# Kernel tuning notes

Measured on AMD Instinct MI355X. Metric: run time of the kernel, lower is better.

The kernel has to match this reference:

```python
import jax, jax.numpy as jnp
import numpy as np

NEG_BIG = -9e15


def setup_inputs() -> dict:
    key = jax.random.key(0)
    k1, k2, k3, k4 = jax.random.split(key, 4)
    B, N, F_in, F_out = 8, 2048, 512, 256
    x = jax.random.normal(k1, (B, N, F_in), dtype=jnp.float32)
    adj = jax.random.randint(k2, (B, N, N), 0, 2, dtype=jnp.int32)
    W = jax.random.normal(k3, (F_in, F_out), dtype=jnp.float32) * (1.414 / np.sqrt(F_in))
    a = jax.random.normal(k4, (2 * F_out, 1), dtype=jnp.float32) * 0.1
    return {"x": x, "adj": adj, "W": W, "a": a}


def reference(x, adj, W, a):
    # x: [B,N,Fin], adj: [B,N,N] int mask, W: [Fin,Fout], a: [2*Fout,1]
    alpha = 0.2  # LeakyReLU negative slope
    F_out = W.shape[1]
    h = jnp.einsum('bnf,fo->bno', x, W)              # [B,N,Fout]
    a1 = a[:F_out, 0]                                # [Fout]
    a2 = a[F_out:, 0]                                # [Fout]
    # e_ij = LeakyReLU([h_i || h_j] . a) = LeakyReLU(h_i.a1 + h_j.a2)
    f = h @ a1                                       # [B,N]
    g = h @ a2                                       # [B,N]
    e = jax.nn.leaky_relu(f[:, :, None] + g[:, None, :], negative_slope=alpha)  # [B,N,N]
    e = jnp.where(adj > 0, e, NEG_BIG)
    attention = jax.nn.softmax(e, axis=2)            # row-wise over neighbors j
    h_prime = jnp.einsum('bij,bjo->bio', attention, h)  # [B,N,Fout]
    return jax.nn.elu(h_prime)                       # concat=True path
```

## Files before the change

### kernel.cpp

```cpp
#include <hip/hip_runtime.h>
#include <math.h>

#define BATCH 8
#define NN    2048
#define FIN   512
#define FOUT  256
#define NEG_BIG -9000000000000000.0f

typedef __attribute__((ext_vector_type(8))) short bf16x8;
typedef __attribute__((ext_vector_type(4))) float f32x4;

__device__ __forceinline__ unsigned short f2bf(float x) {
    unsigned u = __float_as_uint(x);
    u = (u + 0x7FFF + ((u >> 16) & 1)) >> 16;
    return (unsigned short)u;
}
__device__ __forceinline__ float bf2f(unsigned short h) {
    return __uint_as_float(((unsigned)h) << 16);
}
__device__ __forceinline__ void gload_lds16(const void* g, void* l) {
    __builtin_amdgcn_global_load_lds((const __attribute__((address_space(1))) void*)g,
                                     (__attribute__((address_space(3))) void*)l,
                                     16, 0, 0);
}

__global__ __launch_bounds__(256) void wt_prep(const float* __restrict__ W,
                                               unsigned short* __restrict__ Wt_hi,
                                               unsigned short* __restrict__ Wt_lo) {
    const int tg = blockIdx.x * 256 + threadIdx.x;
    const int n  = tg >> 7;
    const int k4 = (tg & 127) * 4;
    unsigned short h[4], lo[4];
    #pragma unroll
    for (int i = 0; i < 4; i++) {
        const float v = W[(size_t)(k4 + i) * FOUT + n];
        h[i]  = f2bf(v);
        lo[i] = f2bf(v - bf2f(h[i]));
    }
    uint2 ph, pl;
    ph.x = h[0]  | ((unsigned)h[1]  << 16); ph.y = h[2]  | ((unsigned)h[3]  << 16);
    pl.x = lo[0] | ((unsigned)lo[1] << 16); pl.y = lo[2] | ((unsigned)lo[3] << 16);
    *(uint2*)(Wt_hi + (size_t)n * FIN + k4) = ph;
    *(uint2*)(Wt_lo + (size_t)n * FIN + k4) = pl;
}

__global__ __launch_bounds__(256, 2) void gemm_xw(const float* __restrict__ x,
        const unsigned short* __restrict__ Wt_hi,
        const unsigned short* __restrict__ Wt_lo,
        unsigned short* __restrict__ ht_hi,
        unsigned short* __restrict__ ht_lo) {
    __shared__ unsigned short As_hi[128][40];
    __shared__ unsigned short As_lo[128][40];
    __shared__ __attribute__((aligned(16))) unsigned short Tr[64][136];
    const int t  = threadIdx.x;
    const int m0 = (blockIdx.x >> 2) * 128;
    const int n0 = (blockIdx.x & 3) * 64;
    const int l  = t & 63, w = t >> 6;
    const int wr = w >> 1, wc = w & 1;
    const int lr = l & 15, lk = l >> 4;

    f32x4 acc[4][2];
    #pragma unroll
    for (int mt = 0; mt < 4; mt++)
        #pragma unroll
        for (int nt = 0; nt < 2; nt++) acc[mt][nt] = (f32x4){0.f,0.f,0.f,0.f};

    for (int k0 = 0; k0 < FIN; k0 += 32) {
        float4 xv[4];
        #pragma unroll
        for (int r = 0; r < 4; r++) {
            const int fidx = t + 256*r, m = fidx >> 3, kq = fidx & 7;
            xv[r] = *(const float4*)(x + (size_t)(m0 + m) * FIN + k0 + kq*4);
        }
        bf16x8 bh[2], bl[2];
        #pragma unroll
        for (int nt = 0; nt < 2; nt++) {
            const size_t off = (size_t)(n0 + wc*32 + nt*16 + lr) * FIN + k0 + lk*8;
            bh[nt] = *(const bf16x8*)(Wt_hi + off);
            bl[nt] = *(const bf16x8*)(Wt_lo + off);
        }
        __syncthreads();
        #pragma unroll
        for (int r = 0; r < 4; r++) {
            const int fidx = t + 256*r, m = fidx >> 3, kq = fidx & 7;
            const float vv[4] = {xv[r].x, xv[r].y, xv[r].z, xv[r].w};
            unsigned short h[4], lo[4];
            #pragma unroll
            for (int i = 0; i < 4; i++) { h[i] = f2bf(vv[i]); lo[i] = f2bf(vv[i] - bf2f(h[i])); }
            uint2 ph, pl;
            ph.x = h[0]  | ((unsigned)h[1]  << 16); ph.y = h[2]  | ((unsigned)h[3]  << 16);
            pl.x = lo[0] | ((unsigned)lo[1] << 16); pl.y = lo[2] | ((unsigned)lo[3] << 16);
            *(uint2*)&As_hi[m][kq*4] = ph;
            *(uint2*)&As_lo[m][kq*4] = pl;
        }
        __syncthreads();
        bf16x8 ah[4], al[4];
        #pragma unroll
        for (int mt = 0; mt < 4; mt++) {
            const int row = wr*64 + mt*16 + lr;
            ah[mt] = *(const bf16x8*)&As_hi[row][lk*8];
            al[mt] = *(const bf16x8*)&As_lo[row][lk*8];
        }
        #pragma unroll
        for (int nt = 0; nt < 2; nt++)
            #pragma unroll
            for (int mt = 0; mt < 4; mt++)
                acc[mt][nt] = __builtin_amdgcn_mfma_f32_16x16x32_bf16(ah[mt], bh[nt], acc[mt][nt], 0, 0, 0);
        #pragma unroll
        for (int nt = 0; nt < 2; nt++)
            #pragma unroll
            for (int mt = 0; mt < 4; mt++)
                acc[mt][nt] = __builtin_amdgcn_mfma_f32_16x16x32_bf16(ah[mt], bl[nt], acc[mt][nt], 0, 0, 0);
        #pragma unroll
        for (int nt = 0; nt < 2; nt++)
            #pragma unroll
            for (int mt = 0; mt < 4; mt++)
                acc[mt][nt] = __builtin_amdgcn_mfma_f32_16x16x32_bf16(al[mt], bh[nt], acc[mt][nt], 0, 0, 0);
    }

    const int bb  = m0 >> 11;
    const int jj0 = m0 & 2047;
    for (int pass = 0; pass < 2; pass++) {
        #pragma unroll
        for (int mt = 0; mt < 4; mt++)
            #pragma unroll
            for (int nt = 0; nt < 2; nt++) {
                const int nl = wc*32 + nt*16 + lr;
                const int ml = wr*64 + mt*16 + lk*4;
                const float vv[4] = {acc[mt][nt].x, acc[mt][nt].y, acc[mt][nt].z, acc[mt][nt].w};
                unsigned short s[4];
                #pragma unroll
                for (int r = 0; r < 4; r++) {
                    const unsigned short hh = f2bf(vv[r]);
                    s[r] = pass ? f2bf(vv[r] - bf2f(hh)) : hh;
                }
                *(unsigned*)&Tr[nl][ml]     = s[0] | ((unsigned)s[1] << 16);
                *(unsigned*)&Tr[nl][ml + 2] = s[2] | ((unsigned)s[3] << 16);
            }
        __syncthreads();
        unsigned short* dst = pass ? ht_lo : ht_hi;
        #pragma unroll
        for (int q = 0; q < 4; q++) {
            const int idx = t + 256*q, row = idx >> 4, c = idx & 15;
            *(uint4*)(dst + ((size_t)(bb * FOUT + n0 + row)) * NN + jj0 + c*8) =
                *(const uint4*)&Tr[row][c*8];
        }
        __syncthreads();
    }
}

__global__ __launch_bounds__(256) void fg2(const unsigned short* __restrict__ ht_hi,
                                           const unsigned short* __restrict__ ht_lo,
                                           const float* __restrict__ a,
                                           float* __restrict__ f, float* __restrict__ g) {
    const int lane  = threadIdx.x & 63;
    const int chunk = blockIdx.x * 4 + (threadIdx.x >> 6);
    const int b  = chunk >> 5;
    const int jw = (chunk & 31) * 64 + lane;
    const size_t base = (size_t)b * FOUT * NN + jw;
    float fs = 0.f, gs = 0.f;
    #pragma unroll 4
    for (int n = 0; n < FOUT; n++) {
        const float hv = bf2f(ht_hi[base + (size_t)n * NN]) + bf2f(ht_lo[base + (size_t)n * NN]);
        fs = fmaf(hv, a[n], fs);
        gs = fmaf(hv, a[FOUT + n], gs);
    }
    f[b * NN + jw] = fs;
    g[b * NN + jw] = gs;
}

__global__ __launch_bounds__(512, 1) void gat_attn(
        const unsigned short* __restrict__ ht_hi,
        const unsigned short* __restrict__ ht_lo,
        const int* __restrict__ adj,
        const float* __restrict__ f, const float* __restrict__ g,
        float* __restrict__ out) {
    __shared__ __attribute__((aligned(16))) unsigned short Hs_hi[256*64];
    __shared__ __attribute__((aligned(16))) unsigned short Hs_lo[256*64];
    __shared__ __attribute__((aligned(16))) unsigned short Ps_hi[64*64];
    __shared__ __attribute__((aligned(16))) unsigned short Ps_lo[64*64];
    __shared__ __attribute__((aligned(16))) float m_s[64];
    __shared__ __attribute__((aligned(16))) float l_s[64];
    __shared__ __attribute__((aligned(16))) float fac_s[64];

    const int b  = blockIdx.x & 7;
    const int i0 = (blockIdx.x >> 3) * 64;
    const int t  = threadIdx.x;
    const int w  = t >> 6, l = t & 63;
    const int lr = l & 15, lk = l >> 4;
    const int wr = w >> 2, wc = w & 3;
    const int ar = t >> 3, jg = t & 7;

    const float fi = f[b * NN + i0 + ar];
    if (t < 64) { m_s[t] = -INFINITY; l_s[t] = 0.f; }

    f32x4 acc[2][4];
    #pragma unroll
    for (int mt = 0; mt < 2; mt++)
        #pragma unroll
        for (int nt = 0; nt < 4; nt++) acc[mt][nt] = (f32x4){0.f,0.f,0.f,0.f};

    const unsigned short* hb_hi = ht_hi + (size_t)b * FOUT * NN;
    const unsigned short* hb_lo = ht_lo + (size_t)b * FOUT * NN;
    const size_t arow = ((size_t)b * NN + i0 + ar) * NN + jg * 8;
    const float* grow = g + b * NN + jg * 8;

    int4   adjA = *(const int4*)(adj + arow);
    int4   adjB = *(const int4*)(adj + arow + 4);
    float4 gA   = *(const float4*)(grow);
    float4 gB   = *(const float4*)(grow + 4);

    const int sidx = w * 4;

    for (int jt = 0; jt < 32; jt++) {
        __syncthreads();

        const int j0 = jt * 64;
        #pragma unroll
        for (int q = 0; q < 4; q++) {
            const int idx = (sidx + q) * 64 + l;
            const int n = idx >> 3, c = idx & 7;
            const int cc = c ^ (n & 7);
            const size_t go = (size_t)n * NN + j0 + cc * 8;
            gload_lds16(hb_hi + go, &Hs_hi[(sidx + q) * 512]);
            gload_lds16(hb_lo + go, &Hs_lo[(sidx + q) * 512]);
        }

        {
            float s[8];
            {
                const float v0 = fi + gA.x, v1 = fi + gA.y, v2 = fi + gA.z, v3 = fi + gA.w;
                const float v4 = fi + gB.x, v5 = fi + gB.y, v6 = fi + gB.z, v7 = fi + gB.w;
                s[0] = adjA.x > 0 ? (v0 > 0.f ? v0 : 0.2f*v0) : NEG_BIG;
                s[1] = adjA.y > 0 ? (v1 > 0.f ? v1 : 0.2f*v1) : NEG_BIG;
                s[2] = adjA.z > 0 ? (v2 > 0.f ? v2 : 0.2f*v2) : NEG_BIG;
                s[3] = adjA.w > 0 ? (v3 > 0.f ? v3 : 0.2f*v3) : NEG_BIG;
                s[4] = adjB.x > 0 ? (v4 > 0.f ? v4 : 0.2f*v4) : NEG_BIG;
                s[5] = adjB.y > 0 ? (v5 > 0.f ? v5 : 0.2f*v5) : NEG_BIG;
                s[6] = adjB.z > 0 ? (v6 > 0.f ? v6 : 0.2f*v6) : NEG_BIG;
                s[7] = adjB.w > 0 ? (v7 > 0.f ? v7 : 0.2f*v7) : NEG_BIG;
            }
            float mloc = s[0];
            #pragma unroll
            for (int e = 1; e < 8; e++) mloc = fmaxf(mloc, s[e]);
            mloc = fmaxf(mloc, __shfl_xor(mloc, 1));
            mloc = fmaxf(mloc, __shfl_xor(mloc, 2));
            mloc = fmaxf(mloc, __shfl_xor(mloc, 4));
            const float m_old = m_s[ar];
            const float m_new = fmaxf(m_old, mloc);
            float p[8], rs = 0.f;
            #pragma unroll
            for (int e = 0; e < 8; e++) { p[e] = __expf(s[e] - m_new); rs += p[e]; }
            rs += __shfl_xor(rs, 1);
            rs += __shfl_xor(rs, 2);
            rs += __shfl_xor(rs, 4);
            if (jg == 0) {
                const float fac = __expf(m_old - m_new);
                fac_s[ar] = fac;
                l_s[ar]   = l_s[ar] * fac + rs;
                m_s[ar]   = m_new;
            }
            unsigned ph[4], pl[4];
            #pragma unroll
            for (int e = 0; e < 8; e += 2) {
                const unsigned short h0 = f2bf(p[e]),   h1 = f2bf(p[e+1]);
                const unsigned short q0 = f2bf(p[e] - bf2f(h0));
                const unsigned short q1 = f2bf(p[e+1] - bf2f(h1));
                ph[e >> 1] = h0 | ((unsigned)h1 << 16);
                pl[e >> 1] = q0 | ((unsigned)q1 << 16);
            }
            const int cs = (jg ^ (ar & 7)) * 8;
            *(uint4*)&Ps_hi[ar * 64 + cs] = make_uint4(ph[0], ph[1], ph[2], ph[3]);
            *(uint4*)&Ps_lo[ar * 64 + cs] = make_uint4(pl[0], pl[1], pl[2], pl[3]);
        }
        __syncthreads();

        if (jt + 1 < 32) {
            const size_t o = (size_t)(jt + 1) * 64;
            adjA = *(const int4*)(adj + arow + o);
            adjB = *(const int4*)(adj + arow + o + 4);
            gA   = *(const float4*)(grow + o);
            gB   = *(const float4*)(grow + o + 4);
        }

        #pragma unroll
        for (int mt = 0; mt < 2; mt++) {
            const f32x4 fac4 = *(const f32x4*)&fac_s[wr*32 + mt*16 + lk*4];
            #pragma unroll
            for (int nt = 0; nt < 4; nt++) acc[mt][nt] *= fac4;
        }
        #pragma unroll
        for (int kt = 0; kt < 2; kt++) {
            bf16x8 ah[2], al[2], bh[4], bl[4];
            #pragma unroll
            for (int mt = 0; mt < 2; mt++) {
                const int row = wr*32 + mt*16 + lr;
                const int cs  = ((kt*4 + lk) ^ (row & 7)) * 8;
                ah[mt] = *(const bf16x8*)&Ps_hi[row * 64 + cs];
                al[mt] = *(const bf16x8*)&Ps_lo[row * 64 + cs];
            }
            #pragma unroll
            for (int nt = 0; nt < 4; nt++) {
                const int n  = wc*64 + nt*16 + lr;
                const int cs = ((kt*4 + lk) ^ (n & 7)) * 8;
                bh[nt] = *(const bf16x8*)&Hs_hi[n * 64 + cs];
                bl[nt] = *(const bf16x8*)&Hs_lo[n * 64 + cs];
            }
            #pragma unroll
            for (int nt = 0; nt < 4; nt++)
                #pragma unroll
                for (int mt = 0; mt < 2; mt++)
                    acc[mt][nt] = __builtin_amdgcn_mfma_f32_16x16x32_bf16(ah[mt], bh[nt], acc[mt][nt], 0, 0, 0);
            #pragma unroll
            for (int nt = 0; nt < 4; nt++)
                #pragma unroll
                for (int mt = 0; mt < 2; mt++)
                    acc[mt][nt] = __builtin_amdgcn_mfma_f32_16x16x32_bf16(ah[mt], bl[nt], acc[mt][nt], 0, 0, 0);
            #pragma unroll
            for (int nt = 0; nt < 4; nt++)
                #pragma unroll
                for (int mt = 0; mt < 2; mt++)
                    acc[mt][nt] = __builtin_amdgcn_mfma_f32_16x16x32_bf16(al[mt], bh[nt], acc[mt][nt], 0, 0, 0);
        }
    }

    __syncthreads();
    #pragma unroll
    for (int mt = 0; mt < 2; mt++) {
        const f32x4 lv = *(const f32x4*)&l_s[wr*32 + mt*16 + lk*4];
        const float linv[4] = {1.f/lv.x, 1.f/lv.y, 1.f/lv.z, 1.f/lv.w};
        #pragma unroll
        for (int nt = 0; nt < 4; nt++) {
            const int n = wc*64 + nt*16 + lr;
            const float av[4] = {acc[mt][nt].x, acc[mt][nt].y, acc[mt][nt].z, acc[mt][nt].w};
            #pragma unroll
            for (int r = 0; r < 4; r++) {
                float v = av[r] * linv[r];
                v = v > 0.f ? v : (__expf(v) - 1.f);
                out[((size_t)(b * NN + i0 + wr*32 + mt*16 + lk*4 + r)) * FOUT + n] = v;
            }
        }
    }
}

extern "C" void kernel_launch(void* const* d_in, const int* in_sizes, int n_in,
                              void* d_out, int out_size, void* d_ws, size_t ws_size,
                              hipStream_t stream) {
    const float* x   = (const float*)d_in[0];
    const int*   adj = (const int*)  d_in[1];
    const float* W   = (const float*)d_in[2];
    const float* a   = (const float*)d_in[3];
    float* outp = (float*)d_out;

    char* ws = (char*)d_ws;
    unsigned short* ht_hi = (unsigned short*)ws;                       ws += (size_t)BATCH*FOUT*NN*2;
    unsigned short* ht_lo = (unsigned short*)ws;                       ws += (size_t)BATCH*FOUT*NN*2;
    unsigned short* Wt_hi = (unsigned short*)ws;                       ws += (size_t)FOUT*FIN*2;
    unsigned short* Wt_lo = (unsigned short*)ws;                       ws += (size_t)FOUT*FIN*2;
    float* f = (float*)ws;                                             ws += (size_t)BATCH*NN*4;
    float* g = (float*)ws;

    wt_prep <<<128, 256, 0, stream>>>(W, Wt_hi, Wt_lo);
    gemm_xw <<<512, 256, 0, stream>>>(x, Wt_hi, Wt_lo, ht_hi, ht_lo);
    fg2     <<<64,  256, 0, stream>>>(ht_hi, ht_lo, a, f, g);
    gat_attn<<<256, 512, 0, stream>>>(ht_hi, ht_lo, adj, f, g, outp);
}
```

Baseline: 320.5 us.

## Compute softmax probabilities in MFMA registers and double-buffer H tiles

The attention kernel now has each wave compute the masked LeakyReLU scores and online-softmax probabilities directly in the MFMA A-operand register layout. This removes the P tile in shared memory, the shared max/sum/scale arrays and one barrier per tile. The H tile is double-buffered so the next tile's global-to-LDS load overlaps current compute, and adjacency/g loads are prefetched. The fg2 kernel splits the feature reduction across four waves with an LDS combine and launches more blocks for parallelism. Each of the four waves sharing a row block now redundantly computes the same probabilities and reads the same adjacency rows, which adds ALU work and adj traffic.

```diff
diff --git a/kernel.cpp b/kernel.cpp
--- a/kernel.cpp
+++ b/kernel.cpp
@@ -153,20 +153,25 @@
                                            const unsigned short* __restrict__ ht_lo,
                                            const float* __restrict__ a,
                                            float* __restrict__ f, float* __restrict__ g) {
-    const int lane  = threadIdx.x & 63;
-    const int chunk = blockIdx.x * 4 + (threadIdx.x >> 6);
+    __shared__ float Fp[4][64], Gp[4][64];
+    const int lane = threadIdx.x & 63, wv = threadIdx.x >> 6;
+    const int chunk = blockIdx.x;
     const int b  = chunk >> 5;
     const int jw = (chunk & 31) * 64 + lane;
     const size_t base = (size_t)b * FOUT * NN + jw;
     float fs = 0.f, gs = 0.f;
     #pragma unroll 4
-    for (int n = 0; n < FOUT; n++) {
+    for (int n = wv*64; n < wv*64 + 64; n++) {
         const float hv = bf2f(ht_hi[base + (size_t)n * NN]) + bf2f(ht_lo[base + (size_t)n * NN]);
         fs = fmaf(hv, a[n], fs);
         gs = fmaf(hv, a[FOUT + n], gs);
     }
-    f[b * NN + jw] = fs;
-    g[b * NN + jw] = gs;
+    Fp[wv][lane] = fs; Gp[wv][lane] = gs;
+    __syncthreads();
+    if (wv == 0) {
+        f[b * NN + jw] = Fp[0][lane] + Fp[1][lane] + Fp[2][lane] + Fp[3][lane];
+        g[b * NN + jw] = Gp[0][lane] + Gp[1][lane] + Gp[2][lane] + Gp[3][lane];
+    }
 }
 
 __global__ __launch_bounds__(512, 1) void gat_attn(
@@ -175,13 +180,8 @@
         const int* __restrict__ adj,
         const float* __restrict__ f, const float* __restrict__ g,
         float* __restrict__ out) {
-    __shared__ __attribute__((aligned(16))) unsigned short Hs_hi[256*64];
-    __shared__ __attribute__((aligned(16))) unsigned short Hs_lo[256*64];
-    __shared__ __attribute__((aligned(16))) unsigned short Ps_hi[64*64];
-    __shared__ __attribute__((aligned(16))) unsigned short Ps_lo[64*64];
-    __shared__ __attribute__((aligned(16))) float m_s[64];
-    __shared__ __attribute__((aligned(16))) float l_s[64];
-    __shared__ __attribute__((aligned(16))) float fac_s[64];
+    __shared__ __attribute__((aligned(16))) unsigned short Hs_hi[2][16384];
+    __shared__ __attribute__((aligned(16))) unsigned short Hs_lo[2][16384];
 
     const int b  = blockIdx.x & 7;
     const int i0 = (blockIdx.x >> 3) * 64;
@@ -189,153 +189,161 @@
     const int w  = t >> 6, l = t & 63;
     const int lr = l & 15, lk = l >> 4;
     const int wr = w >> 2, wc = w & 3;
-    const int ar = t >> 3, jg = t & 7;
-
-    const float fi = f[b * NN + i0 + ar];
-    if (t < 64) { m_s[t] = -INFINITY; l_s[t] = 0.f; }
-
-    f32x4 acc[2][4];
-    #pragma unroll
-    for (int mt = 0; mt < 2; mt++)
-        #pragma unroll
-        for (int nt = 0; nt < 4; nt++) acc[mt][nt] = (f32x4){0.f,0.f,0.f,0.f};
 
     const unsigned short* hb_hi = ht_hi + (size_t)b * FOUT * NN;
     const unsigned short* hb_lo = ht_lo + (size_t)b * FOUT * NN;
-    const size_t arow = ((size_t)b * NN + i0 + ar) * NN + jg * 8;
-    const float* grow = g + b * NN + jg * 8;
-
-    int4   adjA = *(const int4*)(adj + arow);
-    int4   adjB = *(const int4*)(adj + arow + 4);
-    float4 gA   = *(const float4*)(grow);
-    float4 gB   = *(const float4*)(grow + 4);
-
-    const int sidx = w * 4;
-
-    for (int jt = 0; jt < 32; jt++) {
-        __syncthreads();
-
+
+    const int rbase = i0 + wr*32 + lr;
+    const float fi0 = f[b*NN + rbase];
+    const float fi1 = f[b*NN + rbase + 16];
+    const int* adjr0 = adj + ((size_t)(b*NN + rbase)) * NN;
+    const int* adjr1 = adjr0 + (size_t)16 * NN;
+    const float* gb = g + b*NN;
+
+    float m_reg[2] = {-INFINITY, -INFINITY};
+    float l_reg[2] = {0.f, 0.f};
+    f32x4 acc[2][4] = {};
+
+    const int slot = w * 4;
+
+    int4   ap[2][2][2];
+    float4 gp[2][2];
+
+    auto STAGE = [&](int jt, int buf) {
         const int j0 = jt * 64;
         #pragma unroll
         for (int q = 0; q < 4; q++) {
-            const int idx = (sidx + q) * 64 + l;
+            const int idx = (slot + q) * 64 + l;
             const int n = idx >> 3, c = idx & 7;
             const int cc = c ^ (n & 7);
             const size_t go = (size_t)n * NN + j0 + cc * 8;
-            gload_lds16(hb_hi + go, &Hs_hi[(sidx + q) * 512]);
-            gload_lds16(hb_lo + go, &Hs_lo[(sidx + q) * 512]);
-        }
-
-        {
-            float s[8];
-            {
-                const float v0 = fi + gA.x, v1 = fi + gA.y, v2 = fi + gA.z, v3 = fi + gA.w;
-                const float v4 = fi + gB.x, v5 = fi + gB.y, v6 = fi + gB.z, v7 = fi + gB.w;
-                s[0] = adjA.x > 0 ? (v0 > 0.f ? v0 : 0.2f*v0) : NEG_BIG;
-                s[1] = adjA.y > 0 ? (v1 > 0.f ? v1 : 0.2f*v1) : NEG_BIG;
-                s[2] = adjA.z > 0 ? (v2 > 0.f ? v2 : 0.2f*v2) : NEG_BIG;
-                s[3] = adjA.w > 0 ? (v3 > 0.f ? v3 : 0.2f*v3) : NEG_BIG;
-                s[4] = adjB.x > 0 ? (v4 > 0.f ? v4 : 0.2f*v4) : NEG_BIG;
-                s[5] = adjB.y > 0 ? (v5 > 0.f ? v5 : 0.2f*v5) : NEG_BIG;
-                s[6] = adjB.z > 0 ? (v6 > 0.f ? v6 : 0.2f*v6) : NEG_BIG;
-                s[7] = adjB.w > 0 ? (v7 > 0.f ? v7 : 0.2f*v7) : NEG_BIG;
-            }
-            float mloc = s[0];
-            #pragma unroll
-            for (int e = 1; e < 8; e++) mloc = fmaxf(mloc, s[e]);
-            mloc = fmaxf(mloc, __shfl_xor(mloc, 1));
-            mloc = fmaxf(mloc, __shfl_xor(mloc, 2));
-            mloc = fmaxf(mloc, __shfl_xor(mloc, 4));
-            const float m_old = m_s[ar];
-            const float m_new = fmaxf(m_old, mloc);
-            float p[8], rs = 0.f;
-            #pragma unroll
-            for (int e = 0; e < 8; e++) { p[e] = __expf(s[e] - m_new); rs += p[e]; }
-            rs += __shfl_xor(rs, 1);
-            rs += __shfl_xor(rs, 2);
-            rs += __shfl_xor(rs, 4);
-            if (jg == 0) {
-                const float fac = __expf(m_old - m_new);
-                fac_s[ar] = fac;
-                l_s[ar]   = l_s[ar] * fac + rs;
-                m_s[ar]   = m_new;
-            }
-            unsigned ph[4], pl[4];
-            #pragma unroll
-            for (int e = 0; e < 8; e += 2) {
-                const unsigned short h0 = f2bf(p[e]),   h1 = f2bf(p[e+1]);
-                const unsigned short q0 = f2bf(p[e] - bf2f(h0));
-                const unsigned short q1 = f2bf(p[e+1] - bf2f(h1));
-                ph[e >> 1] = h0 | ((unsigned)h1 << 16);
-                pl[e >> 1] = q0 | ((unsigned)q1 << 16);
-            }
-            const int cs = (jg ^ (ar & 7)) * 8;
-            *(uint4*)&Ps_hi[ar * 64 + cs] = make_uint4(ph[0], ph[1], ph[2], ph[3]);
-            *(uint4*)&Ps_lo[ar * 64 + cs] = make_uint4(pl[0], pl[1], pl[2], pl[3]);
-        }
-        __syncthreads();
-
-        if (jt + 1 < 32) {
-            const size_t o = (size_t)(jt + 1) * 64;
-            adjA = *(const int4*)(adj + arow + o);
-            adjB = *(const int4*)(adj + arow + o + 4);
-            gA   = *(const float4*)(grow + o);
-            gB   = *(const float4*)(grow + o + 4);
-        }
-
+            gload_lds16(hb_hi + go, &Hs_hi[buf][(slot + q) * 512]);
+            gload_lds16(hb_lo + go, &Hs_lo[buf][(slot + q) * 512]);
+        }
+    };
+    auto LOADAG = [&](int jt) {
+        const int j0 = jt * 64;
+        #pragma unroll
+        for (int kt = 0; kt < 2; kt++) {
+            const int jo = j0 + kt*32 + lk*8;
+            gp[kt][0]    = *(const float4*)(gb + jo);
+            gp[kt][1]    = *(const float4*)(gb + jo + 4);
+            ap[0][kt][0] = *(const int4*)(adjr0 + jo);
+            ap[0][kt][1] = *(const int4*)(adjr0 + jo + 4);
+            ap[1][kt][0] = *(const int4*)(adjr1 + jo);
+            ap[1][kt][1] = *(const int4*)(adjr1 + jo + 4);
+        }
+    };
+
+    STAGE(0, 0);
+    LOADAG(0);
+
+    for (int jt = 0; jt < 32; jt++) {
+        const int buf = jt & 1;
+        __syncthreads();
+        if (jt + 1 < 32) STAGE(jt + 1, buf ^ 1);
+
+        bf16x8 ph[2][2], pl[2][2];
+        float fac[2];
         #pragma unroll
         for (int mt = 0; mt < 2; mt++) {
-            const f32x4 fac4 = *(const f32x4*)&fac_s[wr*32 + mt*16 + lk*4];
-            #pragma unroll
-            for (int nt = 0; nt < 4; nt++) acc[mt][nt] *= fac4;
-        }
+            const float fi = mt ? fi1 : fi0;
+            float p[2][8];
+            float mloc = -INFINITY;
+            #pragma unroll
+            for (int kt = 0; kt < 2; kt++) {
+                const float gv[8] = {gp[kt][0].x, gp[kt][0].y, gp[kt][0].z, gp[kt][0].w,
+                                     gp[kt][1].x, gp[kt][1].y, gp[kt][1].z, gp[kt][1].w};
+                const int av[8] = {ap[mt][kt][0].x, ap[mt][kt][0].y, ap[mt][kt][0].z, ap[mt][kt][0].w,
+                                   ap[mt][kt][1].x, ap[mt][kt][1].y, ap[mt][kt][1].z, ap[mt][kt][1].w};
+                #pragma unroll
+                for (int e = 0; e < 8; e++) {
+                    const float v = fi + gv[e];
+                    const float s = av[e] > 0 ? (v > 0.f ? v : 0.2f * v) : NEG_BIG;
+                    p[kt][e] = s;
+                    mloc = fmaxf(mloc, s);
+                }
+            }
+            mloc = fmaxf(mloc, __shfl_xor(mloc, 16));
+            mloc = fmaxf(mloc, __shfl_xor(mloc, 32));
+            const float mn = fmaxf(m_reg[mt], mloc);
+            float rs = 0.f;
+            #pragma unroll
+            for (int kt = 0; kt < 2; kt++)
+                #pragma unroll
+                for (int e = 0; e < 8; e++) { p[kt][e] = __expf(p[kt][e] - mn); rs += p[kt][e]; }
+            rs += __shfl_xor(rs, 16);
+            rs += __shfl_xor(rs, 32);
+            fac[mt]   = __expf(m_reg[mt] - mn);
+            l_reg[mt] = l_reg[mt] * fac[mt] + rs;
+            m_reg[mt] = mn;
+            #pragma unroll
+            for (int kt = 0; kt < 2; kt++) {
+                unsigned hw[4], lw[4];
+                #pragma unroll
+                for (int e = 0; e < 8; e += 2) {
+                    const unsigned short h0 = f2bf(p[kt][e]),   h1 = f2bf(p[kt][e+1]);
+                    const unsigned short q0 = f2bf(p[kt][e]   - bf2f(h0));
+                    const unsigned short q1 = f2bf(p[kt][e+1] - bf2f(h1));
+                    hw[e >> 1] = h0 | ((unsigned)h1 << 16);
+                    lw[e >> 1] = q0 | ((unsigned)q1 << 16);
+                }
+                ph[mt][kt] = (bf16x8)__builtin_bit_cast(bf16x8, make_uint4(hw[0], hw[1], hw[2], hw[3]));
+                pl[mt][kt] = (bf16x8)__builtin_bit_cast(bf16x8, make_uint4(lw[0], lw[1], lw[2], lw[3]));
+            }
+        }
+
+        if (jt + 1 < 32) LOADAG(jt + 1);
+
+        #pragma unroll
+        for (int mt = 0; mt < 2; mt++) {
+            f32x4 f4;
+            #pragma unroll
+            for (int r = 0; r < 4; r++) f4[r] = __shfl(fac[mt], lk*4 + r);
+            #pragma unroll
+            for (int nt = 0; nt < 4; nt++) acc[mt][nt] *= f4;
+        }
+
         #pragma unroll
         for (int kt = 0; kt < 2; kt++) {
-            bf16x8 ah[2], al[2], bh[4], bl[4];
-            #pragma unroll
-            for (int mt = 0; mt < 2; mt++) {
-                const int row = wr*32 + mt*16 + lr;
-                const int cs  = ((kt*4 + lk) ^ (row & 7)) * 8;
-                ah[mt] = *(const bf16x8*)&Ps_hi[row * 64 + cs];
-                al[mt] = *(const bf16x8*)&Ps_lo[row * 64 + cs];
-            }
+            bf16x8 bh[4], bl[4];
             #pragma unroll
             for (int nt = 0; nt < 4; nt++) {
                 const int n  = wc*64 + nt*16 + lr;
                 const int cs = ((kt*4 + lk) ^ (n & 7)) * 8;
-                bh[nt] = *(const bf16x8*)&Hs_hi[n * 64 + cs];
-                bl[nt] = *(const bf16x8*)&Hs_lo[n * 64 + cs];
+                bh[nt] = *(const bf16x8*)&Hs_hi[buf][n * 64 + cs];
+                bl[nt] = *(const bf16x8*)&Hs_lo[buf][n * 64 + cs];
             }
             #pragma unroll
             for (int nt = 0; nt < 4; nt++)
                 #pragma unroll
                 for (int mt = 0; mt < 2; mt++)
-                    acc[mt][nt] = __builtin_amdgcn_mfma_f32_16x16x32_bf16(ah[mt], bh[nt], acc[mt][nt], 0, 0, 0);
+                    acc[mt][nt] = __builtin_amdgcn_mfma_f32_16x16x32_bf16(ph[mt][kt], bh[nt], acc[mt][nt], 0, 0, 0);
             #pragma unroll
             for (int nt = 0; nt < 4; nt++)
                 #pragma unroll
                 for (int mt = 0; mt < 2; mt++)
-                    acc[mt][nt] = __builtin_amdgcn_mfma_f32_16x16x32_bf16(ah[mt], bl[nt], acc[mt][nt], 0, 0, 0);
+                    acc[mt][nt] = __builtin_amdgcn_mfma_f32_16x16x32_bf16(ph[mt][kt], bl[nt], acc[mt][nt], 0, 0, 0);
             #pragma unroll
             for (int nt = 0; nt < 4; nt++)
                 #pragma unroll
                 for (int mt = 0; mt < 2; mt++)
-                    acc[mt][nt] = __builtin_amdgcn_mfma_f32_16x16x32_bf16(al[mt], bh[nt], acc[mt][nt], 0, 0, 0);
-        }
-    }
-
-    __syncthreads();
+                    acc[mt][nt] = __builtin_amdgcn_mfma_f32_16x16x32_bf16(pl[mt][kt], bh[nt], acc[mt][nt], 0, 0, 0);
+        }
+    }
+
     #pragma unroll
     for (int mt = 0; mt < 2; mt++) {
-        const f32x4 lv = *(const f32x4*)&l_s[wr*32 + mt*16 + lk*4];
-        const float linv[4] = {1.f/lv.x, 1.f/lv.y, 1.f/lv.z, 1.f/lv.w};
+        float li[4];
+        #pragma unroll
+        for (int r = 0; r < 4; r++) li[r] = 1.f / __shfl(l_reg[mt], lk*4 + r);
         #pragma unroll
         for (int nt = 0; nt < 4; nt++) {
             const int n = wc*64 + nt*16 + lr;
             const float av[4] = {acc[mt][nt].x, acc[mt][nt].y, acc[mt][nt].z, acc[mt][nt].w};
             #pragma unroll
             for (int r = 0; r < 4; r++) {
-                float v = av[r] * linv[r];
+                float v = av[r] * li[r];
                 v = v > 0.f ? v : (__expf(v) - 1.f);
                 out[((size_t)(b * NN + i0 + wr*32 + mt*16 + lk*4 + r)) * FOUT + n] = v;
             }
@@ -362,6 +370,6 @@
 
     wt_prep <<<128, 256, 0, stream>>>(W, Wt_hi, Wt_lo);
     gemm_xw <<<512, 256, 0, stream>>>(x, Wt_hi, Wt_lo, ht_hi, ht_lo);
-    fg2     <<<64,  256, 0, stream>>>(ht_hi, ht_lo, a, f, g);
+    fg2     <<<256, 256, 0, stream>>>(ht_hi, ht_lo, a, f, g);
     gat_attn<<<256, 512, 0, stream>>>(ht_hi, ht_lo, adj, f, g, outp);
 }
```

New measurement: 349.6 us. 1.09x slower.
